# Kernel optimization log

Hardware: AMD Instinct MI355X
Metric: run time of the kernel (lower is better)

## Reference

```python
import jax, jax.numpy as jnp
import numpy as np

E = 64       # expert_nums
D = 32       # embed_dim
H = 4        # num_heads
HD = D // H  # head_dim = 8
B = 524288
TOP_K = 2
NOISE_EPS = 0.01


def setup_inputs() -> dict:
    key = jax.random.key(0)
    ks = jax.random.split(key, 10)
    return {
        "taskID": jax.random.randint(ks[0], (B,), 0, 6),
        "embed_table": jax.random.normal(ks[1], (6, D), jnp.float32),
        "expert_keys": jax.random.normal(ks[2], (D, D), jnp.float32),
        "in_proj_w": jax.random.normal(ks[3], (3 * D, D), jnp.float32) * 0.1,
        "in_proj_b": jax.random.normal(ks[4], (3 * D,), jnp.float32) * 0.1,
        "fc_gate_w": jax.random.normal(ks[5], (E, D), jnp.float32) * 0.1,
        "fc_gate_b": jax.random.normal(ks[6], (E,), jnp.float32) * 0.1,
        "fc_noise_w": jax.random.normal(ks[7], (E, D), jnp.float32) * 0.1,
        "fc_noise_b": jax.random.normal(ks[8], (E,), jnp.float32) * 0.1,
        "noise": jax.random.normal(ks[9], (B, E), jnp.float32),
    }


def reference(taskID, embed_table, expert_keys, in_proj_w, in_proj_b,
              fc_gate_w, fc_gate_b, fc_noise_w, fc_noise_b, noise):
    bsz = taskID.shape[0]
    x = embed_table[taskID]                                   # [B, D] task embeddings (query)
    # nn.MultiheadAttention q/k projections (v and out_proj don't affect attn_weights)
    Wq, Wk = in_proj_w[:D], in_proj_w[D:2 * D]
    bq, bk = in_proj_b[:D], in_proj_b[D:2 * D]
    Q = (x @ Wq.T + bq).reshape(bsz, H, HD)                   # [B, H, HD]
    K = (expert_keys @ Wk.T + bk).reshape(D, H, HD)           # [S=32, H, HD], shared across batch
    scores = jnp.einsum('bhd,shd->bhs', Q, K) / np.sqrt(HD).astype(np.float32)
    attn_w = jax.nn.softmax(scores, axis=-1).mean(axis=1)     # averaged over heads -> [B, 32]
    expert_weight = jax.nn.softmax(attn_w, axis=-1)           # module re-applies softmax (faithful)
    clean_logits = expert_weight @ fc_gate_w.T + fc_gate_b    # [B, E]
    noise_std = jax.nn.softplus(expert_weight @ fc_noise_w.T + fc_noise_b) + NOISE_EPS
    logits = clean_logits + noise * noise_std                 # train=True path
    top_logits, top_indices = jax.lax.top_k(logits, min(TOP_K + 1, E))
    tk_logits = top_logits[:, :TOP_K]                         # [B, TOP_K]
    tk_indices = top_indices[:, :TOP_K]
    tk_gates = jax.nn.softmax(tk_logits, axis=-1)
    rows = jnp.arange(bsz)[:, None]
    gates = jnp.zeros_like(logits).at[rows, tk_indices].set(tk_gates)  # scatter sparse gates
    load = gates.sum(axis=0)                                  # [E]
    return gates, load
```

## Files before the change

### kernel.cpp

```cpp
#include <hip/hip_runtime.h>
#include <math.h>

#define NE 64
#define NTASK 6
#define BLK 256
#define TILE 256

__global__ void precompute_kernel(
    const float* __restrict__ embed_table,
    const float* __restrict__ expert_keys,
    const float* __restrict__ in_proj_w,
    const float* __restrict__ in_proj_b,
    const float* __restrict__ fc_gate_w,
    const float* __restrict__ fc_gate_b,
    const float* __restrict__ fc_noise_w,
    const float* __restrict__ fc_noise_b,
    float*   __restrict__ tab_f,
    double2* __restrict__ tab_d,
    float*   __restrict__ load)
{
    __shared__ double Ksh[32][32];
    __shared__ double Qsh[6][32];
    __shared__ double sc[24][32];
    __shared__ double attn[6][32];
    __shared__ double ew[6][32];
    __shared__ double red[24];
    __shared__ double red2[6];
    const int tid = threadIdx.x;

    if (tid < NE) load[tid] = 0.f;

    for (int idx = tid; idx < 32 * 32; idx += BLK) {
        int s = idx >> 5, j = idx & 31;
        double acc = (double)in_proj_b[32 + j];
        for (int d = 0; d < 32; ++d)
            acc += (double)expert_keys[s * 32 + d] * (double)in_proj_w[(32 + j) * 32 + d];
        Ksh[s][j] = acc;
    }
    for (int idx = tid; idx < NTASK * 32; idx += BLK) {
        int t = idx >> 5, j = idx & 31;
        double acc = (double)in_proj_b[j];
        for (int d = 0; d < 32; ++d)
            acc += (double)embed_table[t * 32 + d] * (double)in_proj_w[j * 32 + d];
        Qsh[t][j] = acc;
    }
    __syncthreads();

    const double SCALE = 1.0 / (double)((float)2.8284271247461903);
    for (int idx = tid; idx < 24 * 32; idx += BLK) {
        int th = idx >> 5, s = idx & 31;
        int t = th >> 2, h = th & 3;
        double acc = 0.0;
        for (int d = 0; d < 8; ++d)
            acc += Qsh[t][h * 8 + d] * Ksh[s][h * 8 + d];
        sc[th][s] = acc * SCALE;
    }
    __syncthreads();
    if (tid < 24) {
        double m = sc[tid][0];
        for (int s = 1; s < 32; ++s) m = fmax(m, sc[tid][s]);
        red[tid] = m;
    }
    __syncthreads();
    for (int idx = tid; idx < 24 * 32; idx += BLK) {
        int th = idx >> 5, s = idx & 31;
        sc[th][s] = exp(sc[th][s] - red[th]);
    }
    __syncthreads();
    if (tid < 24) {
        double sum = 0.0;
        for (int s = 0; s < 32; ++s) sum += sc[tid][s];
        red[tid] = 1.0 / sum;
    }
    __syncthreads();
    for (int idx = tid; idx < NTASK * 32; idx += BLK) {
        int t = idx >> 5, s = idx & 31;
        attn[t][s] = 0.25 * (sc[t*4+0][s]*red[t*4+0] + sc[t*4+1][s]*red[t*4+1]
                           + sc[t*4+2][s]*red[t*4+2] + sc[t*4+3][s]*red[t*4+3]);
    }
    __syncthreads();
    if (tid < NTASK) {
        double m = attn[tid][0];
        for (int s = 1; s < 32; ++s) m = fmax(m, attn[tid][s]);
        red2[tid] = m;
    }
    __syncthreads();
    for (int idx = tid; idx < NTASK * 32; idx += BLK) {
        int t = idx >> 5, s = idx & 31;
        ew[t][s] = exp(attn[t][s] - red2[t]);
    }
    __syncthreads();
    if (tid < NTASK) {
        double sum = 0.0;
        for (int s = 0; s < 32; ++s) sum += ew[tid][s];
        red2[tid] = 1.0 / sum;
    }
    __syncthreads();

    for (int idx = tid; idx < NTASK * NE; idx += BLK) {
        int t = idx >> 6, e = idx & 63;
        double inv = red2[t];
        double a  = (double)fc_gate_b[e];
        double n0 = (double)fc_noise_b[e];
        for (int d = 0; d < 32; ++d) {
            double w = ew[t][d] * inv;
            a  += w * (double)fc_gate_w [e * 32 + d];
            n0 += w * (double)fc_noise_w[e * 32 + d];
        }
        double sp = (n0 > 0.0) ? (n0 + log1p(exp(-n0))) : log1p(exp(n0));
        double ns = sp + 0.01;
        const int o = e * 8 + t;
        tab_f[o * 2 + 0] = (float)a;
        tab_f[o * 2 + 1] = (float)ns;
        tab_d[o] = make_double2(a, ns);
    }
    for (int idx = tid; idx < 512; idx += BLK) {
        if ((idx & 7) >= NTASK) {
            tab_f[idx * 2 + 0] = 0.f;
            tab_f[idx * 2 + 1] = 0.f;
            tab_d[idx] = make_double2(0.0, 0.0);
        }
    }
}

__global__ __launch_bounds__(BLK) void router_kernel(
    const int*     __restrict__ taskID,
    const float*   __restrict__ noise,
    const float*   __restrict__ tab_f,
    const double2* __restrict__ tab_d,
    float* __restrict__ gates,
    float* __restrict__ load,
    int B)
{
    __shared__ float4  tile[TILE * 16];
    __shared__ float2  s_tabf[512];
    __shared__ double2 s_tabd[512];
    __shared__ float   s_load[NE];

    const int tid = threadIdx.x;
    const long long rowBase = (long long)blockIdx.x * TILE;
    const int b = (int)(rowBase + tid);
    int t = 0;
    if (b < B) t = taskID[b];

    {
        const float2* gf = (const float2*)tab_f;
        for (int i = tid; i < 512; i += BLK) {
            s_tabf[i] = gf[i];
            s_tabd[i] = tab_d[i];
        }
    }
    if (tid < NE) s_load[tid] = 0.f;

    const float4* gsrc = (const float4*)noise + rowBase * 16;
    #pragma unroll
    for (int k = 0; k < 16; ++k) {
        const int f = tid + k * BLK;
        const int row = f >> 4, c = f & 15;
        float4 v = make_float4(0.f, 0.f, 0.f, 0.f);
        if (rowBase + row < B) v = gsrc[f];
        tile[row * 16 + (c ^ (row & 15))] = v;
    }
    __syncthreads();

    if (b < B) {
        const int sw = tid & 15;
        float4* myrow = &tile[tid * 16];

        float v1 = -INFINITY, v2 = -INFINITY, v3 = -INFINITY;
        int   i1 = 0, i2 = 0, i3 = 0;
        float n1 = 0.f, n2 = 0.f, n3 = 0.f;

        #pragma unroll
        for (int c = 0; c < 16; ++c) {
            const float4 nv = myrow[c ^ sw];
            const float na[4] = {nv.x, nv.y, nv.z, nv.w};
            #pragma unroll
            for (int j = 0; j < 4; ++j) {
                const int e = c * 4 + j;
                const float2 cn = s_tabf[e * 8 + t];
                const float l = __fadd_rn(cn.x, __fmul_rn(na[j], cn.y));
                if (l > v1) {
                    v3 = v2; i3 = i2; n3 = n2;
                    v2 = v1; i2 = i1; n2 = n1;
                    v1 = l;  i1 = e;  n1 = na[j];
                } else if (l > v2) {
                    v3 = v2; i3 = i2; n3 = n2;
                    v2 = l;  i2 = e;  n2 = na[j];
                } else if (l > v3) {
                    v3 = l;  i3 = e;  n3 = na[j];
                }
            }
        }

        double2 ca = s_tabd[i1 * 8 + t]; double va = ca.x + (double)n1 * ca.y; int ia = i1;
        double2 cb = s_tabd[i2 * 8 + t]; double vb = cb.x + (double)n2 * cb.y; int ib = i2;
        double2 cc = s_tabd[i3 * 8 + t]; double vc = cc.x + (double)n3 * cc.y; int ic = i3;
        if (vb > va || (vb == va && ib < ia)) { double tv = va; va = vb; vb = tv; int ti = ia; ia = ib; ib = ti; }
        if (vc > va || (vc == va && ic < ia)) { double tv = va; va = vc; vc = tv; int ti = ia; ia = ic; ic = ti; }
        if (vc > vb || (vc == vb && ic < ib)) { double tv = vb; vb = vc; vc = tv; int ti = ib; ib = ic; ic = ti; }

        const double e2 = exp(vb - va);
        const double denom = 1.0 + e2;
        const float g1 = (float)(1.0 / denom);
        const float g2 = (float)(e2 / denom);

        #pragma unroll
        for (int c = 0; c < 16; ++c) {
            const int e0 = c * 4;
            float4 w;
            w.x = (e0 + 0 == ia) ? g1 : ((e0 + 0 == ib) ? g2 : 0.f);
            w.y = (e0 + 1 == ia) ? g1 : ((e0 + 1 == ib) ? g2 : 0.f);
            w.z = (e0 + 2 == ia) ? g1 : ((e0 + 2 == ib) ? g2 : 0.f);
            w.w = (e0 + 3 == ia) ? g1 : ((e0 + 3 == ib) ? g2 : 0.f);
            myrow[c ^ sw] = w;
        }
        atomicAdd(&s_load[ia], g1);
        atomicAdd(&s_load[ib], g2);
    }
    __syncthreads();

    float4* gdst = (float4*)gates + rowBase * 16;
    #pragma unroll
    for (int k = 0; k < 16; ++k) {
        const int f = tid + k * BLK;
        const int row = f >> 4, c = f & 15;
        if (rowBase + row < B) gdst[f] = tile[row * 16 + (c ^ (row & 15))];
    }
    if (tid < NE) atomicAdd(&load[tid], s_load[tid]);
}

extern "C" void kernel_launch(void* const* d_in, const int* in_sizes, int n_in,
                              void* d_out, int out_size, void* d_ws, size_t ws_size,
                              hipStream_t stream) {
    const int*   taskID      = (const int*)  d_in[0];
    const float* embed_table = (const float*)d_in[1];
    const float* expert_keys = (const float*)d_in[2];
    const float* in_proj_w   = (const float*)d_in[3];
    const float* in_proj_b   = (const float*)d_in[4];
    const float* fc_gate_w   = (const float*)d_in[5];
    const float* fc_gate_b   = (const float*)d_in[6];
    const float* fc_noise_w  = (const float*)d_in[7];
    const float* fc_noise_b  = (const float*)d_in[8];
    const float* noise       = (const float*)d_in[9];

    const int B = in_sizes[0];

    float*   tab_f = (float*)d_ws;
    double2* tab_d = (double2*)((char*)d_ws + 4096);

    float* gates = (float*)d_out;
    float* load  = gates + (size_t)B * NE;

    precompute_kernel<<<1, BLK, 0, stream>>>(embed_table, expert_keys, in_proj_w, in_proj_b,
                                             fc_gate_w, fc_gate_b, fc_noise_w, fc_noise_b,
                                             tab_f, tab_d, load);

    const int grid = (B + TILE - 1) / TILE;
    router_kernel<<<grid, BLK, 0, stream>>>(taskID, noise, tab_f, tab_d,
                                            gates, load, B);
}
```

Before: 139.8 us.

## Split each row across four lanes with shuffle top-3 merge and persistent grid

The router kernel now assigns each batch row to four lanes, each handling 16 experts, and merges the per-lane top-3 candidates with xor shuffles, in place of one thread per row. Noise is read straight from global memory and gates are written with nontemporal vector stores, so the shared-memory staging tile goes away. A fixed grid of 2048 blocks loops over row groups. The coefficient table is transposed to task-major order and swizzled to avoid bank conflicts. This is meant to cut LDS traffic and serial per-thread work and raise memory parallelism, at the cost of extra shuffle work and a redundant double-precision refinement in every lane.

```diff
diff --git a/kernel.cpp b/kernel.cpp
--- a/kernel.cpp
+++ b/kernel.cpp
@@ -4,7 +4,10 @@
 #define NE 64
 #define NTASK 6
 #define BLK 256
-#define TILE 256
+#define GRID 2048
+#define RPW 16
+
+typedef float nfloat4 __attribute__((ext_vector_type(4)));
 
 __global__ void precompute_kernel(
     const float* __restrict__ embed_table,
@@ -109,13 +112,13 @@
         }
         double sp = (n0 > 0.0) ? (n0 + log1p(exp(-n0))) : log1p(exp(n0));
         double ns = sp + 0.01;
-        const int o = e * 8 + t;
+        const int o = t * 64 + e;
         tab_f[o * 2 + 0] = (float)a;
         tab_f[o * 2 + 1] = (float)ns;
         tab_d[o] = make_double2(a, ns);
     }
     for (int idx = tid; idx < 512; idx += BLK) {
-        if ((idx & 7) >= NTASK) {
+        if ((idx >> 6) >= NTASK) {
             tab_f[idx * 2 + 0] = 0.f;
             tab_f[idx * 2 + 1] = 0.f;
             tab_d[idx] = make_double2(0.0, 0.0);
@@ -125,108 +128,138 @@
 
 __global__ __launch_bounds__(BLK) void router_kernel(
     const int*     __restrict__ taskID,
-    const float*   __restrict__ noise,
-    const float*   __restrict__ tab_f,
-    const double2* __restrict__ tab_d,
+    const float4*  __restrict__ noise4,
+    const float4*  __restrict__ tabf4,
+    const double2* __restrict__ tabd,
     float* __restrict__ gates,
     float* __restrict__ load,
     int B)
 {
-    __shared__ float4  tile[TILE * 16];
-    __shared__ float2  s_tabf[512];
+    __shared__ float4  s_tabf4[256];
     __shared__ double2 s_tabd[512];
     __shared__ float   s_load[NE];
 
     const int tid = threadIdx.x;
-    const long long rowBase = (long long)blockIdx.x * TILE;
-    const int b = (int)(rowBase + tid);
-    int t = 0;
-    if (b < B) t = taskID[b];
-
-    {
-        const float2* gf = (const float2*)tab_f;
-        for (int i = tid; i < 512; i += BLK) {
-            s_tabf[i] = gf[i];
-            s_tabd[i] = tab_d[i];
-        }
-    }
+    for (int i = tid; i < 256; i += BLK) {
+        const int tt = i >> 5, cc = (i >> 3) & 3, rr = i & 7;
+        const int dst = (i & ~7) | (rr ^ ((2 * cc + tt) & 7));
+        s_tabf4[dst] = tabf4[i];
+    }
+    for (int i = tid; i < 512; i += BLK) s_tabd[i] = tabd[i];
     if (tid < NE) s_load[tid] = 0.f;
-
-    const float4* gsrc = (const float4*)noise + rowBase * 16;
-    #pragma unroll
-    for (int k = 0; k < 16; ++k) {
-        const int f = tid + k * BLK;
-        const int row = f >> 4, c = f & 15;
-        float4 v = make_float4(0.f, 0.f, 0.f, 0.f);
-        if (rowBase + row < B) v = gsrc[f];
-        tile[row * 16 + (c ^ (row & 15))] = v;
-    }
-    __syncthreads();
-
-    if (b < B) {
-        const int sw = tid & 15;
-        float4* myrow = &tile[tid * 16];
+    __syncthreads();
+
+    const int lane  = tid & 63;
+    const int sub   = lane >> 2;
+    const int c     = lane & 3;
+    const int ebase = c * 16;
+    const int W = (blockIdx.x * BLK + tid) >> 6;
+    const int nWaves = GRID * (BLK / 64);
+    const int nGroup = (B + RPW - 1) / RPW;
+
+    for (int g = W; g < nGroup; g += nWaves) {
+        const int row = g * RPW + sub;
+        const bool ok = row < B;
+        int t = 0;
+        if (ok) t = taskID[row];
+        const int nb = row * 16 + c * 4;
+        float4 nz0, nz1, nz2, nz3;
+        if (ok) {
+            nz0 = noise4[nb + 0]; nz1 = noise4[nb + 1];
+            nz2 = noise4[nb + 2]; nz3 = noise4[nb + 3];
+        } else {
+            nz0 = nz1 = nz2 = nz3 = make_float4(0.f, 0.f, 0.f, 0.f);
+        }
+
+        const int x  = (2 * c + t) & 7;
+        const int tb = t * 32 + c * 8;
 
         float v1 = -INFINITY, v2 = -INFINITY, v3 = -INFINITY;
         int   i1 = 0, i2 = 0, i3 = 0;
         float n1 = 0.f, n2 = 0.f, n3 = 0.f;
 
+#define INS(l_, e_, n_) {                                                      \
+        const bool b1 = (l_) > v1, b2 = (l_) > v2, b3 = (l_) > v3;             \
+        v3 = b2 ? v2 : (b3 ? (l_) : v3);                                       \
+        i3 = b2 ? i2 : (b3 ? (e_) : i3);                                       \
+        n3 = b2 ? n2 : (b3 ? (n_) : n3);                                       \
+        v2 = b1 ? v1 : (b2 ? (l_) : v2);                                       \
+        i2 = b1 ? i1 : (b2 ? (e_) : i2);                                       \
+        n2 = b1 ? n1 : (b2 ? (n_) : n2);                                       \
+        v1 = b1 ? (l_) : v1;                                                   \
+        i1 = b1 ? (e_) : i1;                                                   \
+        n1 = b1 ? (n_) : n1; }
+
+#define STEP(r_, nlo_, nhi_) {                                                 \
+        const float4 tv = s_tabf4[tb + ((r_) ^ x)];                            \
+        const float l0 = __fadd_rn(tv.x, __fmul_rn((nlo_), tv.y));             \
+        const float l1 = __fadd_rn(tv.z, __fmul_rn((nhi_), tv.w));             \
+        INS(l0, ebase + 2 * (r_),     (nlo_));                                 \
+        INS(l1, ebase + 2 * (r_) + 1, (nhi_)); }
+
+        STEP(0, nz0.x, nz0.y); STEP(1, nz0.z, nz0.w);
+        STEP(2, nz1.x, nz1.y); STEP(3, nz1.z, nz1.w);
+        STEP(4, nz2.x, nz2.y); STEP(5, nz2.z, nz2.w);
+        STEP(6, nz3.x, nz3.y); STEP(7, nz3.z, nz3.w);
+#undef STEP
+#undef INS
+
         #pragma unroll
-        for (int c = 0; c < 16; ++c) {
-            const float4 nv = myrow[c ^ sw];
-            const float na[4] = {nv.x, nv.y, nv.z, nv.w};
-            #pragma unroll
-            for (int j = 0; j < 4; ++j) {
-                const int e = c * 4 + j;
-                const float2 cn = s_tabf[e * 8 + t];
-                const float l = __fadd_rn(cn.x, __fmul_rn(na[j], cn.y));
-                if (l > v1) {
-                    v3 = v2; i3 = i2; n3 = n2;
-                    v2 = v1; i2 = i1; n2 = n1;
-                    v1 = l;  i1 = e;  n1 = na[j];
-                } else if (l > v2) {
-                    v3 = v2; i3 = i2; n3 = n2;
-                    v2 = l;  i2 = e;  n2 = na[j];
-                } else if (l > v3) {
-                    v3 = l;  i3 = e;  n3 = na[j];
-                }
-            }
-        }
-
-        double2 ca = s_tabd[i1 * 8 + t]; double va = ca.x + (double)n1 * ca.y; int ia = i1;
-        double2 cb = s_tabd[i2 * 8 + t]; double vb = cb.x + (double)n2 * cb.y; int ib = i2;
-        double2 cc = s_tabd[i3 * 8 + t]; double vc = cc.x + (double)n3 * cc.y; int ic = i3;
-        if (vb > va || (vb == va && ib < ia)) { double tv = va; va = vb; vb = tv; int ti = ia; ia = ib; ib = ti; }
-        if (vc > va || (vc == va && ic < ia)) { double tv = va; va = vc; vc = tv; int ti = ia; ia = ic; ic = ti; }
-        if (vc > vb || (vc == vb && ic < ib)) { double tv = vb; vb = vc; vc = tv; int ti = ib; ib = ic; ic = ti; }
-
-        const double e2 = exp(vb - va);
+        for (int m = 1; m <= 2; m <<= 1) {
+            const float w1 = __shfl_xor(v1, m), w2 = __shfl_xor(v2, m), w3 = __shfl_xor(v3, m);
+            const int   j1 = __shfl_xor(i1, m), j2 = __shfl_xor(i2, m), j3 = __shfl_xor(i3, m);
+            const float q1 = __shfl_xor(n1, m), q2 = __shfl_xor(n2, m), q3 = __shfl_xor(n3, m);
+            const bool aw = (v1 > w1) || (v1 == w1 && i1 < j1);
+            const float p1 = aw ? v1 : w1, p2 = aw ? v2 : w2, p3 = aw ? v3 : w3;
+            const int   pi1 = aw ? i1 : j1, pi2 = aw ? i2 : j2, pi3 = aw ? i3 : j3;
+            const float pn1 = aw ? n1 : q1, pn2 = aw ? n2 : q2, pn3 = aw ? n3 : q3;
+            const float u1 = aw ? w1 : v1, u2 = aw ? w2 : v2;
+            const int   ui1 = aw ? j1 : i1, ui2 = aw ? j2 : i2;
+            const float un1 = aw ? q1 : n1, un2 = aw ? q2 : n2;
+            const bool b2 = (p2 > u1) || (p2 == u1 && pi2 < ui1);
+            const bool b3a = (p3 > u1) || (p3 == u1 && pi3 < ui1);
+            const bool b3b = (p2 > u2) || (p2 == u2 && pi2 < ui2);
+            v1 = p1;  i1 = pi1; n1 = pn1;
+            v2 = b2 ? p2 : u1;  i2 = b2 ? pi2 : ui1;  n2 = b2 ? pn2 : un1;
+            v3 = b2 ? (b3a ? p3 : u1) : (b3b ? p2 : u2);
+            i3 = b2 ? (b3a ? pi3 : ui1) : (b3b ? pi2 : ui2);
+            n3 = b2 ? (b3a ? pn3 : un1) : (b3b ? pn2 : un2);
+        }
+
+        const double2 A = s_tabd[t * 64 + i1];
+        const double2 Bt = s_tabd[t * 64 + i2];
+        const double2 Ct = s_tabd[t * 64 + i3];
+        double da = A.x  + (double)n1 * A.y;  int ia = i1;
+        double db = Bt.x + (double)n2 * Bt.y; int ib = i2;
+        double dc = Ct.x + (double)n3 * Ct.y; int ic = i3;
+        if (db > da || (db == da && ib < ia)) { double tv = da; da = db; db = tv; int ti = ia; ia = ib; ib = ti; }
+        if (dc > da || (dc == da && ic < ia)) { double tv = da; da = dc; dc = tv; int ti = ia; ia = ic; ic = ti; }
+        if (dc > db || (dc == db && ic < ib)) { double tv = db; db = dc; dc = tv; int ti = ib; ib = ic; ic = ti; }
+
+        const double e2 = exp(db - da);
         const double denom = 1.0 + e2;
         const float g1 = (float)(1.0 / denom);
         const float g2 = (float)(e2 / denom);
 
-        #pragma unroll
-        for (int c = 0; c < 16; ++c) {
-            const int e0 = c * 4;
-            float4 w;
-            w.x = (e0 + 0 == ia) ? g1 : ((e0 + 0 == ib) ? g2 : 0.f);
-            w.y = (e0 + 1 == ia) ? g1 : ((e0 + 1 == ib) ? g2 : 0.f);
-            w.z = (e0 + 2 == ia) ? g1 : ((e0 + 2 == ib) ? g2 : 0.f);
-            w.w = (e0 + 3 == ia) ? g1 : ((e0 + 3 == ib) ? g2 : 0.f);
-            myrow[c ^ sw] = w;
-        }
-        atomicAdd(&s_load[ia], g1);
-        atomicAdd(&s_load[ib], g2);
-    }
-    __syncthreads();
-
-    float4* gdst = (float4*)gates + rowBase * 16;
-    #pragma unroll
-    for (int k = 0; k < 16; ++k) {
-        const int f = tid + k * BLK;
-        const int row = f >> 4, c = f & 15;
-        if (rowBase + row < B) gdst[f] = tile[row * 16 + (c ^ (row & 15))];
-    }
+        if (ok) {
+            nfloat4* gdst = (nfloat4*)(gates + (size_t)nb * 4);
+            #pragma unroll
+            for (int k = 0; k < 4; ++k) {
+                const int e0 = ebase + 4 * k;
+                nfloat4 w;
+                w.x = (e0 + 0 == ia) ? g1 : ((e0 + 0 == ib) ? g2 : 0.f);
+                w.y = (e0 + 1 == ia) ? g1 : ((e0 + 1 == ib) ? g2 : 0.f);
+                w.z = (e0 + 2 == ia) ? g1 : ((e0 + 2 == ib) ? g2 : 0.f);
+                w.w = (e0 + 3 == ia) ? g1 : ((e0 + 3 == ib) ? g2 : 0.f);
+                __builtin_nontemporal_store(w, gdst + k);
+            }
+            if (c == 0) {
+                atomicAdd(&s_load[ia], g1);
+                atomicAdd(&s_load[ib], g2);
+            }
+        }
+    }
+    __syncthreads();
     if (tid < NE) atomicAdd(&load[tid], s_load[tid]);
 }
 
@@ -256,7 +289,7 @@
                                              fc_gate_w, fc_gate_b, fc_noise_w, fc_noise_b,
                                              tab_f, tab_d, load);
 
-    const int grid = (B + TILE - 1) / TILE;
-    router_kernel<<<grid, BLK, 0, stream>>>(taskID, noise, tab_f, tab_d,
+    router_kernel<<<GRID, BLK, 0, stream>>>(taskID, (const float4*)noise,
+                                            (const float4*)tab_f, tab_d,
                                             gates, load, B);
 }
```

Result: slower. 226.4 us (+61.9%).

## Restructure router to 16 lanes per row with shuffle top-2 and persistent grid

Applied to the files above, without the earlier changes.

The router now assigns 16 lanes to each row, one float4 of noise per lane, and merges each lane's top-2 with xor shuffles instead of having one thread scan all 64 experts. It replaces the LDS tile round-trip with direct coalesced global loads and stores, and uses a fixed persistent grid of 2048 blocks that prefetches the next group's noise and task ID. The double-precision re-ranking of the top three candidates is dropped, so ties and near-ties are decided in float only, which could change selections versus the reference. The precompute kernel also stages its weights in shared memory before computing the tables.

```diff
diff --git a/kernel.cpp b/kernel.cpp
--- a/kernel.cpp
+++ b/kernel.cpp
@@ -4,7 +4,7 @@
 #define NE 64
 #define NTASK 6
 #define BLK 256
-#define TILE 256
+#define GRID 2048
 
 __global__ void precompute_kernel(
     const float* __restrict__ embed_table,
@@ -15,10 +15,16 @@
     const float* __restrict__ fc_gate_b,
     const float* __restrict__ fc_noise_w,
     const float* __restrict__ fc_noise_b,
-    float*   __restrict__ tab_f,
-    double2* __restrict__ tab_d,
-    float*   __restrict__ load)
+    float* __restrict__ clg,
+    float* __restrict__ nsg,
+    float* __restrict__ load)
 {
+    __shared__ float s_win[96 * 32];
+    __shared__ float s_wg[64 * 32];
+    __shared__ float s_wn[64 * 32];
+    __shared__ float s_keys[32 * 32];
+    __shared__ float s_emb[6 * 32];
+    __shared__ float s_bin[96], s_bg[64], s_bn[64];
     __shared__ double Ksh[32][32];
     __shared__ double Qsh[6][32];
     __shared__ double sc[24][32];
@@ -30,18 +36,26 @@
 
     if (tid < NE) load[tid] = 0.f;
 
+    for (int i = tid; i < 96 * 32; i += BLK) s_win[i] = in_proj_w[i];
+    for (int i = tid; i < 64 * 32; i += BLK) { s_wg[i] = fc_gate_w[i]; s_wn[i] = fc_noise_w[i]; }
+    for (int i = tid; i < 32 * 32; i += BLK) s_keys[i] = expert_keys[i];
+    for (int i = tid; i < 6 * 32;  i += BLK) s_emb[i] = embed_table[i];
+    if (tid < 96) s_bin[tid] = in_proj_b[tid];
+    if (tid < 64) { s_bg[tid] = fc_gate_b[tid]; s_bn[tid] = fc_noise_b[tid]; }
+    __syncthreads();
+
     for (int idx = tid; idx < 32 * 32; idx += BLK) {
         int s = idx >> 5, j = idx & 31;
-        double acc = (double)in_proj_b[32 + j];
+        double acc = (double)s_bin[32 + j];
         for (int d = 0; d < 32; ++d)
-            acc += (double)expert_keys[s * 32 + d] * (double)in_proj_w[(32 + j) * 32 + d];
+            acc += (double)s_keys[s * 32 + d] * (double)s_win[(32 + j) * 32 + d];
         Ksh[s][j] = acc;
     }
     for (int idx = tid; idx < NTASK * 32; idx += BLK) {
         int t = idx >> 5, j = idx & 31;
-        double acc = (double)in_proj_b[j];
+        double acc = (double)s_bin[j];
         for (int d = 0; d < 32; ++d)
-            acc += (double)embed_table[t * 32 + d] * (double)in_proj_w[j * 32 + d];
+            acc += (double)s_emb[t * 32 + d] * (double)s_win[j * 32 + d];
         Qsh[t][j] = acc;
     }
     __syncthreads();
@@ -100,133 +114,117 @@
     for (int idx = tid; idx < NTASK * NE; idx += BLK) {
         int t = idx >> 6, e = idx & 63;
         double inv = red2[t];
-        double a  = (double)fc_gate_b[e];
-        double n0 = (double)fc_noise_b[e];
+        double a  = (double)s_bg[e];
+        double n0 = (double)s_bn[e];
         for (int d = 0; d < 32; ++d) {
             double w = ew[t][d] * inv;
-            a  += w * (double)fc_gate_w [e * 32 + d];
-            n0 += w * (double)fc_noise_w[e * 32 + d];
+            a  += w * (double)s_wg[e * 32 + d];
+            n0 += w * (double)s_wn[e * 32 + d];
         }
         double sp = (n0 > 0.0) ? (n0 + log1p(exp(-n0))) : log1p(exp(n0));
-        double ns = sp + 0.01;
-        const int o = e * 8 + t;
-        tab_f[o * 2 + 0] = (float)a;
-        tab_f[o * 2 + 1] = (float)ns;
-        tab_d[o] = make_double2(a, ns);
-    }
-    for (int idx = tid; idx < 512; idx += BLK) {
-        if ((idx & 7) >= NTASK) {
-            tab_f[idx * 2 + 0] = 0.f;
-            tab_f[idx * 2 + 1] = 0.f;
-            tab_d[idx] = make_double2(0.0, 0.0);
-        }
+        clg[idx] = (float)a;
+        nsg[idx] = (float)(sp + 0.01);
     }
 }
 
 __global__ __launch_bounds__(BLK) void router_kernel(
-    const int*     __restrict__ taskID,
-    const float*   __restrict__ noise,
-    const float*   __restrict__ tab_f,
-    const double2* __restrict__ tab_d,
-    float* __restrict__ gates,
-    float* __restrict__ load,
+    const int*    __restrict__ taskID,
+    const float4* __restrict__ noise4,
+    const float4* __restrict__ clg4,
+    const float4* __restrict__ nsg4,
+    float4* __restrict__ gates4,
+    float*  __restrict__ load,
     int B)
 {
-    __shared__ float4  tile[TILE * 16];
-    __shared__ float2  s_tabf[512];
-    __shared__ double2 s_tabd[512];
-    __shared__ float   s_load[NE];
+    __shared__ float4 s_cl[96], s_ns[96];
+    __shared__ float  s_load[NE];
 
     const int tid = threadIdx.x;
-    const long long rowBase = (long long)blockIdx.x * TILE;
-    const int b = (int)(rowBase + tid);
-    int t = 0;
-    if (b < B) t = taskID[b];
-
-    {
-        const float2* gf = (const float2*)tab_f;
-        for (int i = tid; i < 512; i += BLK) {
-            s_tabf[i] = gf[i];
-            s_tabd[i] = tab_d[i];
-        }
-    }
+    if (tid < 96) { s_cl[tid] = clg4[tid]; s_ns[tid] = nsg4[tid]; }
     if (tid < NE) s_load[tid] = 0.f;
-
-    const float4* gsrc = (const float4*)noise + rowBase * 16;
-    #pragma unroll
-    for (int k = 0; k < 16; ++k) {
-        const int f = tid + k * BLK;
-        const int row = f >> 4, c = f & 15;
-        float4 v = make_float4(0.f, 0.f, 0.f, 0.f);
-        if (rowBase + row < B) v = gsrc[f];
-        tile[row * 16 + (c ^ (row & 15))] = v;
-    }
-    __syncthreads();
-
-    if (b < B) {
-        const int sw = tid & 15;
-        float4* myrow = &tile[tid * 16];
-
-        float v1 = -INFINITY, v2 = -INFINITY, v3 = -INFINITY;
-        int   i1 = 0, i2 = 0, i3 = 0;
-        float n1 = 0.f, n2 = 0.f, n3 = 0.f;
+    __syncthreads();
+
+    const int lane = tid & 63;
+    const int sl   = lane & 15;
+    const int rsub = lane >> 4;
+    const int e0   = sl * 4;
+    const int W = (blockIdx.x * BLK + tid) >> 6;
+    const int nWaves = GRID * (BLK / 64);
+    const int nG = (B + 3) >> 2;
+    const int n4 = B * 16;
+    const float4 zero4 = make_float4(0.f, 0.f, 0.f, 0.f);
+
+    float4 cur = zero4;
+    int tcur = 0, rowc = 0;
+    if (W < nG) {
+        const int idx = W * 64 + lane;
+        cur = (idx < n4) ? noise4[idx] : zero4;
+        rowc = W * 4 + rsub;
+        tcur = (rowc < B) ? taskID[rowc] : 0;
+    }
+
+    for (int g = W; g < nG; g += nWaves) {
+        const int gn = g + nWaves;
+        float4 nxt = zero4; int tnxt = 0, rown = 0;
+        if (gn < nG) {
+            const int idx = gn * 64 + lane;
+            nxt = (idx < n4) ? noise4[idx] : zero4;
+            rown = gn * 4 + rsub;
+            tnxt = (rown < B) ? taskID[rown] : 0;
+        }
+
+        const float4 c4 = s_cl[tcur * 16 + sl];
+        const float4 s4 = s_ns[tcur * 16 + sl];
+        const float l0 = __fadd_rn(c4.x, __fmul_rn(cur.x, s4.x));
+        const float l1 = __fadd_rn(c4.y, __fmul_rn(cur.y, s4.y));
+        const float l2 = __fadd_rn(c4.z, __fmul_rn(cur.z, s4.z));
+        const float l3 = __fadd_rn(c4.w, __fmul_rn(cur.w, s4.w));
+
+        float v1 = -INFINITY, v2 = -INFINITY;
+        int   i1 = 0, i2 = 0;
+#define INS2(l_, e_) {                                                         \
+        const bool b1_ = (l_) > v1, b2_ = (l_) > v2;                           \
+        v2 = b1_ ? v1 : (b2_ ? (l_) : v2);                                     \
+        i2 = b1_ ? i1 : (b2_ ? (e_) : i2);                                     \
+        v1 = b1_ ? (l_) : v1;                                                  \
+        i1 = b1_ ? (e_) : i1; }
+        INS2(l0, e0 + 0); INS2(l1, e0 + 1); INS2(l2, e0 + 2); INS2(l3, e0 + 3);
+#undef INS2
 
         #pragma unroll
-        for (int c = 0; c < 16; ++c) {
-            const float4 nv = myrow[c ^ sw];
-            const float na[4] = {nv.x, nv.y, nv.z, nv.w};
-            #pragma unroll
-            for (int j = 0; j < 4; ++j) {
-                const int e = c * 4 + j;
-                const float2 cn = s_tabf[e * 8 + t];
-                const float l = __fadd_rn(cn.x, __fmul_rn(na[j], cn.y));
-                if (l > v1) {
-                    v3 = v2; i3 = i2; n3 = n2;
-                    v2 = v1; i2 = i1; n2 = n1;
-                    v1 = l;  i1 = e;  n1 = na[j];
-                } else if (l > v2) {
-                    v3 = v2; i3 = i2; n3 = n2;
-                    v2 = l;  i2 = e;  n2 = na[j];
-                } else if (l > v3) {
-                    v3 = l;  i3 = e;  n3 = na[j];
-                }
-            }
-        }
-
-        double2 ca = s_tabd[i1 * 8 + t]; double va = ca.x + (double)n1 * ca.y; int ia = i1;
-        double2 cb = s_tabd[i2 * 8 + t]; double vb = cb.x + (double)n2 * cb.y; int ib = i2;
-        double2 cc = s_tabd[i3 * 8 + t]; double vc = cc.x + (double)n3 * cc.y; int ic = i3;
-        if (vb > va || (vb == va && ib < ia)) { double tv = va; va = vb; vb = tv; int ti = ia; ia = ib; ib = ti; }
-        if (vc > va || (vc == va && ic < ia)) { double tv = va; va = vc; vc = tv; int ti = ia; ia = ic; ic = ti; }
-        if (vc > vb || (vc == vb && ic < ib)) { double tv = vb; vb = vc; vc = tv; int ti = ib; ib = ic; ic = ti; }
-
-        const double e2 = exp(vb - va);
-        const double denom = 1.0 + e2;
-        const float g1 = (float)(1.0 / denom);
-        const float g2 = (float)(e2 / denom);
-
-        #pragma unroll
-        for (int c = 0; c < 16; ++c) {
-            const int e0 = c * 4;
-            float4 w;
-            w.x = (e0 + 0 == ia) ? g1 : ((e0 + 0 == ib) ? g2 : 0.f);
-            w.y = (e0 + 1 == ia) ? g1 : ((e0 + 1 == ib) ? g2 : 0.f);
-            w.z = (e0 + 2 == ia) ? g1 : ((e0 + 2 == ib) ? g2 : 0.f);
-            w.w = (e0 + 3 == ia) ? g1 : ((e0 + 3 == ib) ? g2 : 0.f);
-            myrow[c ^ sw] = w;
-        }
-        atomicAdd(&s_load[ia], g1);
-        atomicAdd(&s_load[ib], g2);
-    }
-    __syncthreads();
-
-    float4* gdst = (float4*)gates + rowBase * 16;
-    #pragma unroll
-    for (int k = 0; k < 16; ++k) {
-        const int f = tid + k * BLK;
-        const int row = f >> 4, c = f & 15;
-        if (rowBase + row < B) gdst[f] = tile[row * 16 + (c ^ (row & 15))];
-    }
+        for (int m = 1; m <= 8; m <<= 1) {
+            const float w1 = __shfl_xor(v1, m), w2 = __shfl_xor(v2, m);
+            const int   j1 = __shfl_xor(i1, m), j2 = __shfl_xor(i2, m);
+            const bool aw = (v1 > w1) || (v1 == w1 && i1 < j1);
+            const float p1 = aw ? v1 : w1, p2 = aw ? v2 : w2;
+            const int   pi1 = aw ? i1 : j1, pi2 = aw ? i2 : j2;
+            const float u1 = aw ? w1 : v1;
+            const int   ui1 = aw ? j1 : i1;
+            const bool b2 = (p2 > u1) || (p2 == u1 && pi2 < ui1);
+            v1 = p1;  i1 = pi1;
+            v2 = b2 ? p2 : u1;  i2 = b2 ? pi2 : ui1;
+        }
+
+        const float e2x = expf(v2 - v1);
+        const float g1 = 1.0f / (1.0f + e2x);
+        const float g2 = e2x / (1.0f + e2x);
+
+        if (sl == 0 && rowc < B) {
+            atomicAdd(&s_load[i1], g1);
+            atomicAdd(&s_load[i2], g2);
+        }
+
+        float4 w;
+        w.x = (e0 + 0 == i1) ? g1 : ((e0 + 0 == i2) ? g2 : 0.f);
+        w.y = (e0 + 1 == i1) ? g1 : ((e0 + 1 == i2) ? g2 : 0.f);
+        w.z = (e0 + 2 == i1) ? g1 : ((e0 + 2 == i2) ? g2 : 0.f);
+        w.w = (e0 + 3 == i1) ? g1 : ((e0 + 3 == i2) ? g2 : 0.f);
+        const int sidx = g * 64 + lane;
+        if (sidx < n4) gates4[sidx] = w;
+
+        cur = nxt; tcur = tnxt; rowc = rown;
+    }
+    __syncthreads();
     if (tid < NE) atomicAdd(&load[tid], s_load[tid]);
 }
 
@@ -246,17 +244,17 @@
 
     const int B = in_sizes[0];
 
-    float*   tab_f = (float*)d_ws;
-    double2* tab_d = (double2*)((char*)d_ws + 4096);
+    float* clg = (float*)d_ws;
+    float* nsg = clg + 384;
 
     float* gates = (float*)d_out;
     float* load  = gates + (size_t)B * NE;
 
     precompute_kernel<<<1, BLK, 0, stream>>>(embed_table, expert_keys, in_proj_w, in_proj_b,
                                              fc_gate_w, fc_gate_b, fc_noise_w, fc_noise_b,
-                                             tab_f, tab_d, load);
-
-    const int grid = (B + TILE - 1) / TILE;
-    router_kernel<<<grid, BLK, 0, stream>>>(taskID, noise, tab_f, tab_d,
-                                            gates, load, B);
+                                             clg, nsg, load);
+
+    router_kernel<<<GRID, BLK, 0, stream>>>(taskID, (const float4*)noise,
+                                            (const float4*)clg, (const float4*)nsg,
+                                            (float4*)gates, load, B);
 }
```

After: 134.8 us. 1.04x faster.
